# Optimization experiments

Measured on AMD Instinct MI355X. Metric: run time of the kernel, lower is better.

Reference implementation:

```python
import jax, jax.numpy as jnp
import numpy as np

EPS = 1e-5


def _bn(h, gamma, beta):
    # BatchNorm1d, training mode: biased batch statistics over nodes
    mu = jnp.mean(h, axis=0)
    var = jnp.mean(jnp.square(h - mu), axis=0)
    return (h - mu) * jax.lax.rsqrt(var + EPS) * gamma + beta


def setup_inputs() -> dict:
    key = jax.random.key(0)
    ks = jax.random.split(key, 12)
    N, E, D, H = 50000, 800000, 128, 256
    x = jax.random.normal(ks[0], (N, D), dtype=jnp.float32)
    edge_index = jax.random.randint(ks[1], (2, E), 0, N, dtype=jnp.int64)
    train_node_id = jax.random.randint(ks[2], (10000,), 0, N, dtype=jnp.int64)
    def lin(k, fan_in, fan_out):
        bound = 1.0 / np.sqrt(fan_in)
        return jax.random.uniform(k, (fan_in, fan_out), jnp.float32, -bound, bound)
    return {
        "x": x, "edge_index": edge_index, "train_node_id": train_node_id,
        "W1": lin(ks[3], D, H), "b1": jnp.zeros((H,), jnp.float32),
        "W2": lin(ks[4], H, H), "b2": jnp.zeros((H,), jnp.float32),
        "W3": lin(ks[5], H, H), "b3": jnp.zeros((H,), jnp.float32),
        "g1": jnp.ones((H,), jnp.float32), "be1": jnp.zeros((H,), jnp.float32),
        "g2": jnp.ones((H,), jnp.float32), "be2": jnp.zeros((H,), jnp.float32),
        "g3": jnp.ones((H,), jnp.float32), "be3": jnp.zeros((H,), jnp.float32),
        "Wl": lin(ks[6], H, H), "bl": jnp.zeros((H,), jnp.float32),
        "Wf": lin(ks[7], H, 1), "bf": jnp.zeros((1,), jnp.float32),
    }


def reference(x, edge_index, train_node_id, W1, b1, W2, b2, W3, b3,
              g1, be1, g2, be2, g3, be3, Wl, bl, Wf, bf):
    N = x.shape[0]
    loops = jnp.arange(N, dtype=edge_index.dtype)
    row = jnp.concatenate([edge_index[0], loops])  # destinations
    col = jnp.concatenate([edge_index[1], loops])  # sources
    deg = jax.ops.segment_sum(jnp.ones_like(row, dtype=x.dtype), row, num_segments=N)
    d_isqrt = jax.lax.rsqrt(deg)  # deg >= 1 due to self loops
    norm = (d_isqrt[row] * d_isqrt[col])[:, None]  # [E+N, 1]

    def gcn(h, W, b):
        hW = h @ W
        agg = jax.ops.segment_sum(hW[col] * norm, row, num_segments=N)
        return agg + b

    h = jax.nn.relu(_bn(gcn(x, W1, b1), g1, be1))
    h = jax.nn.relu(_bn(gcn(h, W2, b2), g2, be2))
    h = jax.nn.relu(_bn(gcn(h, W3, b3), g3, be3))
    h = jax.nn.relu(h @ Wl + bl)
    h = h[train_node_id]
    return jnp.squeeze(h @ Wf + bf, -1)
```

## Files before the change

### kernel.cpp

```cpp
#include <hip/hip_runtime.h>

typedef unsigned short u16;
typedef __attribute__((ext_vector_type(8))) short short8;
typedef __attribute__((ext_vector_type(4))) float f32x4;

#define CAP 96

#define DEVFN static __device__ __forceinline__

DEVFN float b2f(u16 u) {
    union { float f; unsigned v; } x; x.v = ((unsigned)u) << 16; return x.f;
}
DEVFN u16 f2b(float f) {
    union { float f; unsigned v; } x; x.f = f;
    unsigned r = x.v + 0x7fffu + ((x.v >> 16) & 1u);
    return (u16)(r >> 16);
}

DEVFN int detect64(const int* __restrict__ p) {
    int orv = 0;
#pragma unroll
    for (int i = 1; i < 64; i += 2) orv |= p[i];
    return (orv == 0) ? 1 : 0;
}

DEVFN void accum_row8(short8 v, float* acc) {
    const unsigned* u = (const unsigned*)&v;
#pragma unroll
    for (int k = 0; k < 4; k++) {
        union { float f; unsigned w; } lo, hi;
        lo.w = u[k] << 16;
        hi.w = u[k] & 0xffff0000u;
        acc[2 * k] += lo.f;
        acc[2 * k + 1] += hi.f;
    }
}

__global__ void k_init(const float* __restrict__ W1, const float* __restrict__ W2,
                       const float* __restrict__ W3, const float* __restrict__ Wl,
                       u16* __restrict__ T1, u16* __restrict__ T2,
                       u16* __restrict__ T3, u16* __restrict__ Tl,
                       int* __restrict__ ssrc, float* __restrict__ stat,
                       float* __restrict__ out, int N, int M) {
    int t = blockIdx.x * 256 + threadIdx.x;
    if (t < 229376) {
        const float* W; u16* T; int K; int idx;
        if (t < 32768)        { W = W1; T = T1; K = 128; idx = t; }
        else if (t < 98304)   { W = W2; T = T2; K = 256; idx = t - 32768; }
        else if (t < 163840)  { W = W3; T = T3; K = 256; idx = t - 98304; }
        else                  { W = Wl; T = Tl; K = 256; idx = t - 163840; }
        int k = idx >> 8, n = idx & 255;
        T[(size_t)n * K + k] = f2b(W[(size_t)k * 256 + n]);
    } else if (t < 229376 + 50000) {
        ssrc[(size_t)(t - 229376) * CAP] = 0;
    } else if (t < 229376 + 50000 + 1536) {
        stat[t - 229376 - 50000] = 0.0f;
    } else if (t < 229376 + 50000 + 1536 + 10000) {
        out[t - 229376 - 50000 - 1536] = 0.0f;
    }
}

__global__ void k_fillb(const int* __restrict__ ei, int* __restrict__ ssrc, int E) {
    int fl = detect64(ei);
    int t = blockIdx.x * 256 + threadIdx.x;
    int e0 = t * 2;
    if (e0 >= E) return;
    int r0, r1, c0, c1;
    bool two = (e0 + 1 < E);
    if (fl) {
        const int4* p4 = (const int4*)ei;
        int4 d = p4[t];
        int4 s = p4[(E >> 1) + t];
        r0 = d.x; r1 = d.z; c0 = s.x; c1 = s.z;
    } else {
        const int2* p2 = (const int2*)ei;
        int2 d = p2[t];
        int2 s = p2[(E >> 1) + t];
        r0 = d.x; r1 = d.y; c0 = s.x; c1 = s.y;
    }
    int p0 = atomicAdd(&ssrc[(size_t)r0 * CAP], 1);
    if (p0 < CAP - 1) ssrc[(size_t)r0 * CAP + 1 + p0] = c0;
    if (two) {
        int p1 = atomicAdd(&ssrc[(size_t)r1 * CAP], 1);
        if (p1 < CAP - 1) ssrc[(size_t)r1 * CAP + 1 + p1] = c1;
    }
}

__global__ void k_cvtx(const float* __restrict__ x, const int* __restrict__ ssrc,
                       float* __restrict__ disq, u16* __restrict__ xb, int n) {
    int i = (blockIdx.x * 256 + threadIdx.x) * 4;
    if (i >= n) return;
    int row = i >> 7;
    float d = rsqrtf((float)(ssrc[(size_t)row * CAP] + 1));
    if ((i & 127) == 0) disq[row] = d;
    float4 v = *(const float4*)(x + i);
    ushort4 o;
    o.x = f2b(v.x * d); o.y = f2b(v.y * d); o.z = f2b(v.z * d); o.w = f2b(v.w * d);
    *(ushort4*)(xb + i) = o;
}


template<int KS>
__global__ __launch_bounds__(256, 2) void k_gemm_rb(
        const u16* __restrict__ A, const u16* __restrict__ Wt, u16* __restrict__ C,
        float* __restrict__ Cf, const int* __restrict__ idx,
        int Gtot, float* __restrict__ stat, const float* __restrict__ bias, int relu,
        const float* __restrict__ Wfp, const float* __restrict__ bfp,
        float* __restrict__ outp) {
    constexpr int K = KS * 32;
    __shared__ float sbuf[4][2][64];
    int wv = threadIdx.x >> 6;
    int lane = threadIdx.x & 63;
    int quad = lane >> 4;
    int mr = lane & 15;
    int colbase = blockIdx.y * 64;
    int g0 = blockIdx.x * 16;

    short8 Bf[4][KS];
#pragma unroll
    for (int j = 0; j < 4; j++)
#pragma unroll
        for (int s = 0; s < KS; s++)
            Bf[j][s] = *(const short8*)(Wt + (size_t)(colbase + j * 16 + mr) * K + s * 32 + quad * 8);

    float bv[4] = {0.f, 0.f, 0.f, 0.f};
    if (bias) {
#pragma unroll
        for (int j = 0; j < 4; j++) bv[j] = bias[colbase + j * 16 + mr];
    }
    float wf[4] = {0.f, 0.f, 0.f, 0.f};
    if (Wfp) {
#pragma unroll
        for (int j = 0; j < 4; j++) wf[j] = Wfp[colbase + j * 16 + mr];
    }

    float sreg[4] = {0.f, 0.f, 0.f, 0.f};
    float s2reg[4] = {0.f, 0.f, 0.f, 0.f};
    int f = idx ? detect64(idx) : 0;

    for (int g = wv; g < 16; g += 4) {
        int gg = g0 + g;
        if (gg >= Gtot) continue;
        int row = gg * 16 + mr;
        int arow = idx ? idx[(size_t)row << f] : row;
        const u16* Ap = A + (size_t)arow * K + quad * 8;

        short8 Af[KS];
#pragma unroll
        for (int s = 0; s < KS; s++) Af[s] = *(const short8*)(Ap + s * 32);

        f32x4 acc[4];
#pragma unroll
        for (int j = 0; j < 4; j++) acc[j] = (f32x4){0.f, 0.f, 0.f, 0.f};
#pragma unroll
        for (int s = 0; s < KS; s++)
#pragma unroll
            for (int j = 0; j < 4; j++)
                acc[j] = __builtin_amdgcn_mfma_f32_16x16x32_bf16(Af[s], Bf[j][s], acc[j], 0, 0, 0);

        if (Wfp) {
            float partial[4];
#pragma unroll
            for (int r = 0; r < 4; r++) {
                float pr = 0.f;
#pragma unroll
                for (int j = 0; j < 4; j++) {
                    float v = fmaxf(acc[j][r] + bv[j], 0.f);
                    pr += v * wf[j];
                }
                partial[r] = pr;
            }
#pragma unroll
            for (int r = 0; r < 4; r++) {
                partial[r] += __shfl_xor(partial[r], 1, 64);
                partial[r] += __shfl_xor(partial[r], 2, 64);
                partial[r] += __shfl_xor(partial[r], 4, 64);
                partial[r] += __shfl_xor(partial[r], 8, 64);
            }
            if (mr == 0) {
#pragma unroll
                for (int r = 0; r < 4; r++) {
                    int orow = gg * 16 + quad * 4 + r;
                    float v = partial[r];
                    if (blockIdx.y == 0) v += bfp[0] * 0.25f;
                    atomicAdd(&outp[orow], v);
                }
            }
            continue;
        }

        size_t cb = (size_t)(gg * 16 + quad * 4) * 256 + colbase + mr;
#pragma unroll
        for (int j = 0; j < 4; j++) {
            float s_ = 0.f, s2_ = 0.f;
#pragma unroll
            for (int r = 0; r < 4; r++) {
                float v = acc[j][r];
                s_ += v; s2_ += v * v;
                if (Cf) {
                    Cf[cb + (size_t)r * 256 + j * 16] = v;
                } else {
                    v += bv[j];
                    if (relu) v = fmaxf(v, 0.f);
                    C[cb + (size_t)r * 256 + j * 16] = f2b(v);
                }
            }
            sreg[j] += s_;
            s2reg[j] += s2_;
        }
    }

    if (stat) {
#pragma unroll
        for (int j = 0; j < 4; j++) {
            float s_ = sreg[j], s2_ = s2reg[j];
            s_ += __shfl_xor(s_, 16, 64);  s_ += __shfl_xor(s_, 32, 64);
            s2_ += __shfl_xor(s2_, 16, 64); s2_ += __shfl_xor(s2_, 32, 64);
            if (quad == 0) {
                sbuf[wv][0][j * 16 + mr] = s_;
                sbuf[wv][1][j * 16 + mr] = s2_;
            }
        }
        __syncthreads();
        int t = threadIdx.x;
        if (t < 128) {
            int which = t >> 6, c = t & 63;
            float v = sbuf[0][which][c] + sbuf[1][which][c] +
                      sbuf[2][which][c] + sbuf[3][which][c];
            atomicAdd(&stat[which * 256 + colbase + c], v);
        }
    }
}


__global__ __launch_bounds__(256) void k_gather256(
        const u16* __restrict__ src, const int* __restrict__ ssrc,
        const float* __restrict__ disq, u16* __restrict__ dst, int N) {
    int wave = threadIdx.x >> 6;
    int lane = threadIdx.x & 63;
    int half = lane >> 5;
    int l5 = lane & 31;
    int i = blockIdx.x * 4 + wave;
    if (i >= N) return;
    const u16* base = src + l5 * 8;
    const int* sp = ssrc + (size_t)i * CAP;
    float acc[8] = {0.f, 0.f, 0.f, 0.f, 0.f, 0.f, 0.f, 0.f};
    int e = min(sp[0], CAP - 1);
    int p = 0;
    for (; p + 8 <= e; p += 8) {
        int c0 = sp[1 + p + half];
        int c1 = sp[1 + p + 2 + half];
        int c2 = sp[1 + p + 4 + half];
        int c3 = sp[1 + p + 6 + half];
        short8 v0 = *(const short8*)(base + (size_t)c0 * 256);
        short8 v1 = *(const short8*)(base + (size_t)c1 * 256);
        short8 v2 = *(const short8*)(base + (size_t)c2 * 256);
        short8 v3 = *(const short8*)(base + (size_t)c3 * 256);
        accum_row8(v0, acc);
        accum_row8(v1, acc);
        accum_row8(v2, acc);
        accum_row8(v3, acc);
    }
    for (; p + 2 <= e; p += 2) {
        int c = sp[1 + p + half];
        short8 v = *(const short8*)(base + (size_t)c * 256);
        accum_row8(v, acc);
    }
    {
        int c = half ? i : ((p < e) ? sp[1 + p] : -1);
        if (c >= 0) {
            short8 v = *(const short8*)(base + (size_t)c * 256);
            accum_row8(v, acc);
        }
    }
#pragma unroll
    for (int k = 0; k < 8; k++) acc[k] += __shfl_xor(acc[k], 32, 64);
    if (half == 0) {
        float di = disq[i];
        short8 o;
        u16* op = (u16*)&o;
#pragma unroll
        for (int k = 0; k < 8; k++) op[k] = f2b(acc[k] * di);
        *(short8*)(dst + (size_t)i * 256 + l5 * 8) = o;
    }
}

__global__ __launch_bounds__(256) void k_gather128(
        const u16* __restrict__ src, const int* __restrict__ ssrc,
        const float* __restrict__ disq, u16* __restrict__ dst, int N) {
    int wave = threadIdx.x >> 6;
    int lane = threadIdx.x & 63;
    int q = lane >> 4;
    int l4 = lane & 15;
    int i = blockIdx.x * 4 + wave;
    if (i >= N) return;
    const u16* base = src + l4 * 8;
    const int* sp = ssrc + (size_t)i * CAP;
    float acc[8] = {0.f, 0.f, 0.f, 0.f, 0.f, 0.f, 0.f, 0.f};
    int e = min(sp[0], CAP - 1);
    int p = 0;
    for (; p + 8 <= e; p += 8) {
        int c0 = sp[1 + p + q];
        int c1 = sp[1 + p + 4 + q];
        short8 v0 = *(const short8*)(base + (size_t)c0 * 128);
        short8 v1 = *(const short8*)(base + (size_t)c1 * 128);
        accum_row8(v0, acc);
        accum_row8(v1, acc);
    }
    for (; p + 4 <= e; p += 4) {
        int c = sp[1 + p + q];
        short8 v = *(const short8*)(base + (size_t)c * 128);
        accum_row8(v, acc);
    }
    int rem = e - p;
    {
        int c = (q < rem) ? sp[1 + p + q] : ((q == 3) ? i : -1);
        if (c >= 0) {
            short8 v = *(const short8*)(base + (size_t)c * 128);
            accum_row8(v, acc);
        }
    }
#pragma unroll
    for (int k = 0; k < 8; k++) {
        acc[k] += __shfl_xor(acc[k], 16, 64);
        acc[k] += __shfl_xor(acc[k], 32, 64);
    }
    if (q == 0) {
        float di = disq[i];
        short8 o;
        u16* op = (u16*)&o;
#pragma unroll
        for (int k = 0; k < 8; k++) op[k] = f2b(acc[k] * di);
        *(short8*)(dst + (size_t)i * 128 + l4 * 8) = o;
    }
}


__global__ void k_bnapply(const float* __restrict__ t, const float* __restrict__ stat,
                          const float* __restrict__ gamma, const float* __restrict__ beta,
                          u16* __restrict__ h, int N, float invN,
                          const float* __restrict__ scale) {
    size_t tt = (size_t)blockIdx.x * 256 + threadIdx.x;
    size_t base = tt * 4;
    if (base >= (size_t)N * 256) return;
    int f0 = (int)(base & 255);
    float sc2 = scale ? scale[base >> 8] : 1.0f;
    float4 v = *(const float4*)(t + base);
    float r[4] = {v.x, v.y, v.z, v.w};
    ushort4 o;
    u16* op = (u16*)&o;
#pragma unroll
    for (int j = 0; j < 4; j++) {
        int f = f0 + j;
        float mean = stat[f] * invN;
        float var = stat[256 + f] * invN - mean * mean;
        float rstd = rsqrtf(var + 1e-5f);
        float sc = rstd * gamma[f];
        float sh = beta[f] - mean * sc;
        op[j] = f2b(fmaxf(r[j] * sc + sh, 0.0f) * sc2);
    }
    *(ushort4*)(h + base) = o;
}

__global__ void k_bnapply_idx(const float* __restrict__ t, const float* __restrict__ stat,
                              const float* __restrict__ gamma, const float* __restrict__ beta,
                              const int* __restrict__ idx, u16* __restrict__ zin,
                              int M, float invN) {
    int fl = detect64(idx);
    size_t tt = (size_t)blockIdx.x * 256 + threadIdx.x;
    size_t base = tt * 4;
    if (base >= (size_t)M * 256) return;
    int f0 = (int)(base & 255);
    int row = (int)(base >> 8);
    int node = idx[(size_t)row << fl];
    float4 v = *(const float4*)(t + (size_t)node * 256 + f0);
    float r[4] = {v.x, v.y, v.z, v.w};
    ushort4 o;
    u16* op = (u16*)&o;
#pragma unroll
    for (int j = 0; j < 4; j++) {
        int f = f0 + j;
        float mean = stat[f] * invN;
        float var = stat[256 + f] * invN - mean * mean;
        float rstd = rsqrtf(var + 1e-5f);
        float sc = rstd * gamma[f];
        float sh = beta[f] - mean * sc;
        op[j] = f2b(fmaxf(r[j] * sc + sh, 0.0f));
    }
    *(ushort4*)(zin + (size_t)row * 256 + f0) = o;
}


extern "C" void kernel_launch(void* const* d_in, const int* in_sizes, int n_in,
                              void* d_out, int out_size, void* d_ws, size_t ws_size,
                              hipStream_t stream) {
    const int D = 128, H = 256;
    const int N = in_sizes[0] / D;
    const int E = in_sizes[1] / 2;
    const int M = in_sizes[2];

    const float* x = (const float*)d_in[0];
    const int* ei = (const int*)d_in[1];
    const int* tnid = (const int*)d_in[2];
    const float* W1 = (const float*)d_in[3];
    const float* W2 = (const float*)d_in[5];
    const float* W3 = (const float*)d_in[7];
    const float* g1 = (const float*)d_in[9];
    const float* be1 = (const float*)d_in[10];
    const float* g2 = (const float*)d_in[11];
    const float* be2 = (const float*)d_in[12];
    const float* g3 = (const float*)d_in[13];
    const float* be3 = (const float*)d_in[14];
    const float* Wl = (const float*)d_in[15];
    const float* bl = (const float*)d_in[16];
    const float* Wf = (const float*)d_in[17];
    const float* bfp = (const float*)d_in[18];
    float* out = (float*)d_out;

    char* w = (char*)d_ws;
    size_t off = 0;
    auto carve = [&](size_t bytes) -> void* {
        void* p = w + off;
        off = (off + bytes + 255) & ~(size_t)255;
        return p;
    };

    float* stat = (float*)carve(3 * 512 * 4);
    float* disq = (float*)carve((size_t)N * 4);
    int* ssrc = (int*)carve((size_t)N * CAP * 4);
    u16* Wt1 = (u16*)carve((size_t)H * D * 2);
    u16* Wt2 = (u16*)carve((size_t)H * H * 2);
    u16* Wt3 = (u16*)carve((size_t)H * H * 2);
    u16* Wtl = (u16*)carve((size_t)H * H * 2);
    u16* xb = (u16*)carve((size_t)N * D * 2);
    u16* aggx = (u16*)carve((size_t)N * D * 2);
    u16* aggh = (u16*)carve((size_t)N * H * 2);
    float* tb = (float*)carve((size_t)N * H * 4);
    u16* hb = (u16*)carve((size_t)N * H * 2);
    u16* zin = (u16*)carve((size_t)M * H * 2);

    const float invN = 1.0f / (float)N;

    const int Gn = N / 16;
    const int Gm = M / 16;
    dim3 gemm_grid((Gn + 15) / 16, 4);
    dim3 gemm_grid_m((Gm + 15) / 16, 4);
    const int AB = (N + 3) / 4;
    const int PB = (int)(((size_t)N * H / 4 + 255) / 256);
    const int PBm = (int)(((size_t)M * H / 4 + 255) / 256);

    k_init<<<(229376 + 50000 + 1536 + 10000 + 255) / 256, 256, 0, stream>>>(
        W1, W2, W3, Wl, Wt1, Wt2, Wt3, Wtl, ssrc, stat, out, N, M);
    k_fillb<<<(E / 2 + 255) / 256, 256, 0, stream>>>(ei, ssrc, E);
    k_cvtx<<<(N * D / 4 + 255) / 256, 256, 0, stream>>>(x, ssrc, disq, xb, N * D);

    k_gather128<<<AB, 256, 0, stream>>>(xb, ssrc, disq, aggx, N);
    k_gemm_rb<4><<<gemm_grid, 256, 0, stream>>>(aggx, Wt1, nullptr, tb, nullptr, Gn, stat, nullptr, 0, nullptr, nullptr, nullptr);
    k_bnapply<<<PB, 256, 0, stream>>>(tb, stat, g1, be1, hb, N, invN, disq);
    k_gather256<<<AB, 256, 0, stream>>>(hb, ssrc, disq, aggh, N);
    k_gemm_rb<8><<<gemm_grid, 256, 0, stream>>>(aggh, Wt2, nullptr, tb, nullptr, Gn, stat + 512, nullptr, 0, nullptr, nullptr, nullptr);
    k_bnapply<<<PB, 256, 0, stream>>>(tb, stat + 512, g2, be2, hb, N, invN, disq);
    k_gather256<<<AB, 256, 0, stream>>>(hb, ssrc, disq, aggh, N);
    k_gemm_rb<8><<<gemm_grid, 256, 0, stream>>>(aggh, Wt3, nullptr, tb, nullptr, Gn, stat + 1024, nullptr, 0, nullptr, nullptr, nullptr);
    k_bnapply_idx<<<PBm, 256, 0, stream>>>(tb, stat + 1024, g3, be3, tnid, zin, M, invN);

    k_gemm_rb<8><<<gemm_grid_m, 256, 0, stream>>>(zin, Wtl, nullptr, nullptr, nullptr, Gm, nullptr, bl, 1, Wf, bfp, out);
}
```

Baseline: 459.6 us.

## Store node features in column slices and gather per slice

Node features (xb, hb) and aggregated outputs are now stored in a feature-sliced layout: 8 slices of 16 or 32 bf16 columns each. The gather kernels assign one slice per block, with many neighbors handled per wave and 64B or 32B row segments, and reduce across lanes with shuffles. The GEMM A-load is changed to read this sliced layout. The aim is more memory-level parallelism and smaller, better-packed gather transactions, at the cost of 8x the blocks, repeated neighbor-index reads and extra shuffle reductions. It also fixes the final bias being scaled by 0.25.

```diff
diff --git a/kernel.cpp b/kernel.cpp
--- a/kernel.cpp
+++ b/kernel.cpp
@@ -87,16 +87,18 @@
 }
 
 __global__ void k_cvtx(const float* __restrict__ x, const int* __restrict__ ssrc,
-                       float* __restrict__ disq, u16* __restrict__ xb, int n) {
+                       float* __restrict__ disq, u16* __restrict__ xb, int N) {
     int i = (blockIdx.x * 256 + threadIdx.x) * 4;
-    if (i >= n) return;
+    if (i >= N * 128) return;
     int row = i >> 7;
+    int col = i & 127;
     float d = rsqrtf((float)(ssrc[(size_t)row * CAP] + 1));
-    if ((i & 127) == 0) disq[row] = d;
+    if (col == 0) disq[row] = d;
     float4 v = *(const float4*)(x + i);
     ushort4 o;
     o.x = f2b(v.x * d); o.y = f2b(v.y * d); o.z = f2b(v.z * d); o.w = f2b(v.w * d);
-    *(ushort4*)(xb + i) = o;
+    int slice = col >> 4, within = col & 15;
+    *(ushort4*)(xb + ((size_t)slice * N + row) * 16 + within) = o;
 }
 
 
@@ -104,8 +106,8 @@
 __global__ __launch_bounds__(256, 2) void k_gemm_rb(
         const u16* __restrict__ A, const u16* __restrict__ Wt, u16* __restrict__ C,
         float* __restrict__ Cf, const int* __restrict__ idx,
-        int Gtot, float* __restrict__ stat, const float* __restrict__ bias, int relu,
-        const float* __restrict__ Wfp, const float* __restrict__ bfp,
+        int Gtot, int sliceN, float* __restrict__ stat, const float* __restrict__ bias,
+        int relu, const float* __restrict__ Wfp, const float* __restrict__ bfp,
         float* __restrict__ outp) {
     constexpr int K = KS * 32;
     __shared__ float sbuf[4][2][64];
@@ -143,11 +145,23 @@
         if (gg >= Gtot) continue;
         int row = gg * 16 + mr;
         int arow = idx ? idx[(size_t)row << f] : row;
-        const u16* Ap = A + (size_t)arow * K + quad * 8;
 
         short8 Af[KS];
-#pragma unroll
-        for (int s = 0; s < KS; s++) Af[s] = *(const short8*)(Ap + s * 32);
+        if (sliceN > 0) {
+            if (KS == 8) {
+#pragma unroll
+                for (int s = 0; s < KS; s++)
+                    Af[s] = *(const short8*)(A + ((size_t)s * sliceN + arow) * 32 + quad * 8);
+            } else {
+#pragma unroll
+                for (int s = 0; s < KS; s++)
+                    Af[s] = *(const short8*)(A + ((size_t)(2 * s + (quad >> 1)) * sliceN + arow) * 16 + (quad & 1) * 8);
+            }
+        } else {
+            const u16* Ap = A + (size_t)arow * K + quad * 8;
+#pragma unroll
+            for (int s = 0; s < KS; s++) Af[s] = *(const short8*)(Ap + s * 32);
+        }
 
         f32x4 acc[4];
 #pragma unroll
@@ -182,7 +196,7 @@
                 for (int r = 0; r < 4; r++) {
                     int orow = gg * 16 + quad * 4 + r;
                     float v = partial[r];
-                    if (blockIdx.y == 0) v += bfp[0] * 0.25f;
+                    if (blockIdx.y == 0) v += bfp[0];
                     atomicAdd(&outp[orow], v);
                 }
             }
@@ -233,105 +247,96 @@
 }
 
 
-__global__ __launch_bounds__(256) void k_gather256(
+__global__ __launch_bounds__(256) void k_gather256s(
         const u16* __restrict__ src, const int* __restrict__ ssrc,
         const float* __restrict__ disq, u16* __restrict__ dst, int N) {
     int wave = threadIdx.x >> 6;
     int lane = threadIdx.x & 63;
-    int half = lane >> 5;
-    int l5 = lane & 31;
-    int i = blockIdx.x * 4 + wave;
+    int g = lane >> 2;
+    int l4 = lane & 3;
+    int slice = blockIdx.x & 7;
+    int i = (blockIdx.x >> 3) * 4 + wave;
     if (i >= N) return;
-    const u16* base = src + l5 * 8;
+    const u16* base = src + (size_t)slice * N * 32 + l4 * 8;
     const int* sp = ssrc + (size_t)i * CAP;
+    int e = min(sp[0], CAP - 1);
+    const int* sl = sp + 1;
     float acc[8] = {0.f, 0.f, 0.f, 0.f, 0.f, 0.f, 0.f, 0.f};
-    int e = min(sp[0], CAP - 1);
     int p = 0;
-    for (; p + 8 <= e; p += 8) {
-        int c0 = sp[1 + p + half];
-        int c1 = sp[1 + p + 2 + half];
-        int c2 = sp[1 + p + 4 + half];
-        int c3 = sp[1 + p + 6 + half];
-        short8 v0 = *(const short8*)(base + (size_t)c0 * 256);
-        short8 v1 = *(const short8*)(base + (size_t)c1 * 256);
-        short8 v2 = *(const short8*)(base + (size_t)c2 * 256);
-        short8 v3 = *(const short8*)(base + (size_t)c3 * 256);
-        accum_row8(v0, acc);
-        accum_row8(v1, acc);
-        accum_row8(v2, acc);
-        accum_row8(v3, acc);
-    }
-    for (; p + 2 <= e; p += 2) {
-        int c = sp[1 + p + half];
-        short8 v = *(const short8*)(base + (size_t)c * 256);
+    for (; p + 16 <= e; p += 16) {
+        int c = sl[p + g];
+        short8 v = *(const short8*)(base + (size_t)c * 32);
         accum_row8(v, acc);
     }
+    int rem = e - p;
     {
-        int c = half ? i : ((p < e) ? sp[1 + p] : -1);
+        int c = (g < rem) ? sl[p + g] : ((g == rem) ? i : -1);
         if (c >= 0) {
-            short8 v = *(const short8*)(base + (size_t)c * 256);
+            short8 v = *(const short8*)(base + (size_t)c * 32);
             accum_row8(v, acc);
         }
     }
 #pragma unroll
-    for (int k = 0; k < 8; k++) acc[k] += __shfl_xor(acc[k], 32, 64);
-    if (half == 0) {
+    for (int k = 0; k < 8; k++) {
+        acc[k] += __shfl_xor(acc[k], 4, 64);
+        acc[k] += __shfl_xor(acc[k], 8, 64);
+        acc[k] += __shfl_xor(acc[k], 16, 64);
+        acc[k] += __shfl_xor(acc[k], 32, 64);
+    }
+    if (g == 0) {
         float di = disq[i];
         short8 o;
         u16* op = (u16*)&o;
 #pragma unroll
         for (int k = 0; k < 8; k++) op[k] = f2b(acc[k] * di);
-        *(short8*)(dst + (size_t)i * 256 + l5 * 8) = o;
-    }
-}
-
-__global__ __launch_bounds__(256) void k_gather128(
+        *(short8*)(dst + ((size_t)slice * N + i) * 32 + l4 * 8) = o;
+    }
+}
+
+__global__ __launch_bounds__(256) void k_gather128s(
         const u16* __restrict__ src, const int* __restrict__ ssrc,
         const float* __restrict__ disq, u16* __restrict__ dst, int N) {
     int wave = threadIdx.x >> 6;
     int lane = threadIdx.x & 63;
-    int q = lane >> 4;
-    int l4 = lane & 15;
-    int i = blockIdx.x * 4 + wave;
+    int g = lane >> 1;
+    int l2 = lane & 1;
+    int slice = blockIdx.x & 7;
+    int i = (blockIdx.x >> 3) * 4 + wave;
     if (i >= N) return;
-    const u16* base = src + l4 * 8;
+    const u16* base = src + (size_t)slice * N * 16 + l2 * 8;
     const int* sp = ssrc + (size_t)i * CAP;
+    int e = min(sp[0], CAP - 1);
+    const int* sl = sp + 1;
     float acc[8] = {0.f, 0.f, 0.f, 0.f, 0.f, 0.f, 0.f, 0.f};
-    int e = min(sp[0], CAP - 1);
     int p = 0;
-    for (; p + 8 <= e; p += 8) {
-        int c0 = sp[1 + p + q];
-        int c1 = sp[1 + p + 4 + q];
-        short8 v0 = *(const short8*)(base + (size_t)c0 * 128);
-        short8 v1 = *(const short8*)(base + (size_t)c1 * 128);
-        accum_row8(v0, acc);
-        accum_row8(v1, acc);
-    }
-    for (; p + 4 <= e; p += 4) {
-        int c = sp[1 + p + q];
-        short8 v = *(const short8*)(base + (size_t)c * 128);
+    for (; p + 32 <= e; p += 32) {
+        int c = sl[p + g];
+        short8 v = *(const short8*)(base + (size_t)c * 16);
         accum_row8(v, acc);
     }
     int rem = e - p;
     {
-        int c = (q < rem) ? sp[1 + p + q] : ((q == 3) ? i : -1);
+        int c = (g < rem) ? sl[p + g] : ((g == rem) ? i : -1);
         if (c >= 0) {
-            short8 v = *(const short8*)(base + (size_t)c * 128);
+            short8 v = *(const short8*)(base + (size_t)c * 16);
             accum_row8(v, acc);
         }
     }
 #pragma unroll
     for (int k = 0; k < 8; k++) {
+        acc[k] += __shfl_xor(acc[k], 2, 64);
+        acc[k] += __shfl_xor(acc[k], 4, 64);
+        acc[k] += __shfl_xor(acc[k], 8, 64);
         acc[k] += __shfl_xor(acc[k], 16, 64);
         acc[k] += __shfl_xor(acc[k], 32, 64);
     }
-    if (q == 0) {
+    if (g == 0) {
         float di = disq[i];
         short8 o;
         u16* op = (u16*)&o;
 #pragma unroll
         for (int k = 0; k < 8; k++) op[k] = f2b(acc[k] * di);
-        *(short8*)(dst + (size_t)i * 128 + l4 * 8) = o;
+        *(short8*)(dst + ((size_t)slice * N + i) * 16 + l2 * 8) = o;
     }
 }
 
@@ -344,7 +349,8 @@
     size_t base = tt * 4;
     if (base >= (size_t)N * 256) return;
     int f0 = (int)(base & 255);
-    float sc2 = scale ? scale[base >> 8] : 1.0f;
+    int row = (int)(base >> 8);
+    float sc2 = scale ? scale[row] : 1.0f;
     float4 v = *(const float4*)(t + base);
     float r[4] = {v.x, v.y, v.z, v.w};
     ushort4 o;
@@ -359,7 +365,8 @@
         float sh = beta[f] - mean * sc;
         op[j] = f2b(fmaxf(r[j] * sc + sh, 0.0f) * sc2);
     }
-    *(ushort4*)(h + base) = o;
+    int slice = f0 >> 5, within = f0 & 31;
+    *(ushort4*)(h + ((size_t)slice * N + row) * 32 + within) = o;
 }
 
 __global__ void k_bnapply_idx(const float* __restrict__ t, const float* __restrict__ stat,
@@ -445,24 +452,24 @@
     const int Gm = M / 16;
     dim3 gemm_grid((Gn + 15) / 16, 4);
     dim3 gemm_grid_m((Gm + 15) / 16, 4);
-    const int AB = (N + 3) / 4;
+    const int AGB = ((N + 3) / 4) * 8;
     const int PB = (int)(((size_t)N * H / 4 + 255) / 256);
     const int PBm = (int)(((size_t)M * H / 4 + 255) / 256);
 
     k_init<<<(229376 + 50000 + 1536 + 10000 + 255) / 256, 256, 0, stream>>>(
         W1, W2, W3, Wl, Wt1, Wt2, Wt3, Wtl, ssrc, stat, out, N, M);
     k_fillb<<<(E / 2 + 255) / 256, 256, 0, stream>>>(ei, ssrc, E);
-    k_cvtx<<<(N * D / 4 + 255) / 256, 256, 0, stream>>>(x, ssrc, disq, xb, N * D);
-
-    k_gather128<<<AB, 256, 0, stream>>>(xb, ssrc, disq, aggx, N);
-    k_gemm_rb<4><<<gemm_grid, 256, 0, stream>>>(aggx, Wt1, nullptr, tb, nullptr, Gn, stat, nullptr, 0, nullptr, nullptr, nullptr);
+    k_cvtx<<<(N * D / 4 + 255) / 256, 256, 0, stream>>>(x, ssrc, disq, xb, N);
+
+    k_gather128s<<<AGB, 256, 0, stream>>>(xb, ssrc, disq, aggx, N);
+    k_gemm_rb<4><<<gemm_grid, 256, 0, stream>>>(aggx, Wt1, nullptr, tb, nullptr, Gn, N, stat, nullptr, 0, nullptr, nullptr, nullptr);
     k_bnapply<<<PB, 256, 0, stream>>>(tb, stat, g1, be1, hb, N, invN, disq);
-    k_gather256<<<AB, 256, 0, stream>>>(hb, ssrc, disq, aggh, N);
-    k_gemm_rb<8><<<gemm_grid, 256, 0, stream>>>(aggh, Wt2, nullptr, tb, nullptr, Gn, stat + 512, nullptr, 0, nullptr, nullptr, nullptr);
+    k_gather256s<<<AGB, 256, 0, stream>>>(hb, ssrc, disq, aggh, N);
+    k_gemm_rb<8><<<gemm_grid, 256, 0, stream>>>(aggh, Wt2, nullptr, tb, nullptr, Gn, N, stat + 512, nullptr, 0, nullptr, nullptr, nullptr);
     k_bnapply<<<PB, 256, 0, stream>>>(tb, stat + 512, g2, be2, hb, N, invN, disq);
-    k_gather256<<<AB, 256, 0, stream>>>(hb, ssrc, disq, aggh, N);
-    k_gemm_rb<8><<<gemm_grid, 256, 0, stream>>>(aggh, Wt3, nullptr, tb, nullptr, Gn, stat + 1024, nullptr, 0, nullptr, nullptr, nullptr);
+    k_gather256s<<<AGB, 256, 0, stream>>>(hb, ssrc, disq, aggh, N);
+    k_gemm_rb<8><<<gemm_grid, 256, 0, stream>>>(aggh, Wt3, nullptr, tb, nullptr, Gn, N, stat + 1024, nullptr, 0, nullptr, nullptr, nullptr);
     k_bnapply_idx<<<PBm, 256, 0, stream>>>(tb, stat + 1024, g3, be3, tnid, zin, M, invN);
 
-    k_gemm_rb<8><<<gemm_grid_m, 256, 0, stream>>>(zin, Wtl, nullptr, nullptr, nullptr, Gm, nullptr, bl, 1, Wf, bfp, out);
-}
+    k_gemm_rb<8><<<gemm_grid_m, 256, 0, stream>>>(zin, Wtl, nullptr, nullptr, nullptr, Gm, 0, nullptr, bl, 1, Wf, bfp, out);
+}
```

New measurement: 731.3 us. +59.1%, slower.
